# Kernel tuning notes

Hardware: AMD Instinct MI355X
Metric: run time of the kernel (lower is better)

Reference implementation:

```python
import jax, jax.numpy as jnp
import numpy as np

P, N, D, H, AN, F = 20000, 16, 128, 8, 5, 512
DH = D // H  # 16


def layer_norm(x, g, b, eps=1e-5):
    m = jnp.mean(x, axis=-1, keepdims=True)
    v = jnp.var(x, axis=-1, keepdims=True)
    return (x - m) / jnp.sqrt(v + eps) * g + b


def setup_inputs() -> dict:
    key = jax.random.key(0)
    ks = jax.random.split(key, 12)
    s = 0.02
    return {
        "tgt": jax.random.normal(ks[0], (P, D * AN), jnp.float32),
        "index_pair": jax.random.randint(ks[1], (P, N), 0, P, jnp.int64),
        "cnt": P,
        "dist_atten": jax.random.normal(ks[2], (P, N, H), jnp.float32),
        "Wq": jax.random.normal(ks[3], (D, D), jnp.float32) * s,
        "Wk": jax.random.normal(ks[4], (D, D), jnp.float32) * s,
        "Wo": jax.random.normal(ks[5], (D, D), jnp.float32) * s,
        "W1": jax.random.normal(ks[6], (F, D), jnp.float32) * s,
        "b1f": jnp.zeros((F,), jnp.float32),
        "W2": jax.random.normal(ks[7], (D, F), jnp.float32) * s,
        "b2f": jnp.zeros((D,), jnp.float32),
        "g1": jnp.ones((D,), jnp.float32),
        "be1": jnp.zeros((D,), jnp.float32),
        "g2": jnp.ones((D,), jnp.float32),
        "be2": jnp.zeros((D,), jnp.float32),
    }


def reference(tgt, index_pair, cnt, dist_atten, Wq, Wk, Wo, W1, b1f, W2, b2f, g1, be1, g2, be2):
    x = tgt.reshape(P, D, AN)                       # [P, D, an]
    # Linear applied along D (torch Linear: y = x W^T), acting per equivariant channel an
    q = jnp.einsum('pea,de->pda', x, Wq)
    k = jnp.einsum('pea,de->pda', x, Wk)
    v = jnp.einsum('pea,de->pda', x, Wq)            # source uses to_q for value (faithful)
    # irregular neighbor gather (sa_attention_mapper_v3)
    kg = k.reshape(P, D * AN)[index_pair].reshape(P, N, H, DH, AN)
    vg = v.reshape(P, D * AN)[index_pair].reshape(P, N, H, DH, AN)
    qh = q.reshape(P, H, DH, AN)
    dot = jnp.einsum('phdi,pnhdi->pnh', qh, kg)     # [P, N, H]
    att = jax.nn.softmax((dot + dist_atten) / np.sqrt(DH).astype(np.float32), axis=1)
    t2 = jnp.einsum('pnh,pnhci->phci', att, vg).reshape(P, D, AN)
    t2 = jnp.einsum('pea,de->pda', t2, Wo)
    y = (x + t2).transpose(0, 2, 1)                 # [P, an, D]
    y = layer_norm(y, g1, be1)
    ff = jnp.maximum(y @ W1.T + b1f, 0.0) @ W2.T + b2f
    y = layer_norm(y + ff, g2, be2)
    return y.transpose(0, 2, 1).reshape(P, D * AN)
```

## Files before the change

### kernel.cpp

```cpp
#include <hip/hip_runtime.h>

#define PP   20000
#define NN   16
#define DD   128
#define HH   8
#define ANC  5
#define FF   512
#define PD   640
#define ROWS (PP * ANC)
#define SEG  20480


typedef __attribute__((ext_vector_type(8))) short  bf8;
typedef __attribute__((ext_vector_type(8))) unsigned short ushort8;
typedef __attribute__((ext_vector_type(4))) unsigned short us4;
typedef __attribute__((ext_vector_type(4))) float  f32x4;

__device__ inline float bf2f(unsigned short u) {
  union { unsigned int i; float f; } v; v.i = ((unsigned int)u) << 16; return v.f;
}
__device__ inline unsigned short f2bf(float f) {
  union { float f; unsigned int i; } v; v.f = f;
  unsigned int r = v.i + 0x7FFFu + ((v.i >> 16) & 1u);
  return (unsigned short)(r >> 16);
}

__global__ void k_wconv(const float* __restrict__ Wo, const float* __restrict__ W1,
                        const float* __restrict__ W2, const float* __restrict__ Wq,
                        const float* __restrict__ Wk,
                        unsigned short* __restrict__ Wob, unsigned short* __restrict__ W1b,
                        unsigned short* __restrict__ W2b, unsigned short* __restrict__ Wqb,
                        unsigned short* __restrict__ Wkb)
{
  int i = blockIdx.x * 256 + threadIdx.x;
  if (i < 16384) { Wob[i] = f2bf(Wo[i]); Wqb[i] = f2bf(Wq[i]); Wkb[i] = f2bf(Wk[i]); }
  if (i < 65536) { W1b[i] = f2bf(W1[i]); W2b[i] = f2bf(W2[i]); }
}

__global__ __launch_bounds__(320) void k_xpose(
    const float* __restrict__ tgt, unsigned short* __restrict__ xb)
{
  __shared__ float xs[5 * 1032];
  const int t = threadIdx.x;
  const int p0 = blockIdx.x * 8;
  const float* src = tgt + (size_t)p0 * PD;
#pragma unroll
  for (int i = 0; i < 16; ++i) {
    int lin = t + i * 320;
    float v = src[lin];
    int pt = lin / PD;
    int rem = lin - pt * PD;
    int e = rem / 5;
    int a = rem - e * 5;
    xs[a * 1032 + e * 8 + pt] = v;
  }
  __syncthreads();
  const size_t base = (size_t)(blockIdx.x >> 1) * SEG + (size_t)(blockIdx.x & 1) * 5120;
  for (int i = t; i < 5120; i += 320) {
    int row_l = i >> 7, col = i & 127;
    int pt = row_l / 5, a = row_l - pt * 5;
    xb[base + i] = f2bf(xs[a * 1032 + col * 8 + pt]);
  }
}

__global__ __launch_bounds__(256) void k_qk_gemm(
    const unsigned short* __restrict__ xb, const unsigned short* __restrict__ Wqb,
    const unsigned short* __restrict__ Wkb, unsigned char* __restrict__ kq8,
    unsigned short* __restrict__ qb16)
{
  __shared__ unsigned short Sb[80 * 136];
  const int t = threadIdx.x;
  const int w = t >> 6, l = t & 63;
  const int lc = l & 15, kg = l >> 4;
  const int p0 = blockIdx.x * 16;
  const unsigned short* xseg = xb + (size_t)blockIdx.x * SEG;

  f32x4 zq[5][2], zk[5][2];
#pragma unroll
  for (int m = 0; m < 5; ++m)
#pragma unroll
    for (int n = 0; n < 2; ++n) {
      zq[m][n] = (f32x4){0.f, 0.f, 0.f, 0.f};
      zk[m][n] = (f32x4){0.f, 0.f, 0.f, 0.f};
    }
  bf8 wq[2][4], wk[2][4];
#pragma unroll
  for (int nt = 0; nt < 2; ++nt)
#pragma unroll
    for (int kf = 0; kf < 4; ++kf) {
      size_t wo = (size_t)((2 * w + nt) * 16 + lc) * DD + kf * 32 + kg * 8;
      wq[nt][kf] = *reinterpret_cast<const bf8*>(&Wqb[wo]);
      wk[nt][kf] = *reinterpret_cast<const bf8*>(&Wkb[wo]);
    }
#pragma unroll
  for (int mt = 0; mt < 5; ++mt) {
    const unsigned short* ap = xseg + (mt * 16 + lc) * DD + kg * 8;
    bf8 a0 = *reinterpret_cast<const bf8*>(ap);
    bf8 a1 = *reinterpret_cast<const bf8*>(ap + 32);
    bf8 a2 = *reinterpret_cast<const bf8*>(ap + 64);
    bf8 a3 = *reinterpret_cast<const bf8*>(ap + 96);
#pragma unroll
    for (int nt = 0; nt < 2; ++nt) {
      zq[mt][nt] = __builtin_amdgcn_mfma_f32_16x16x32_bf16(a0, wq[nt][0], zq[mt][nt], 0, 0, 0);
      zq[mt][nt] = __builtin_amdgcn_mfma_f32_16x16x32_bf16(a1, wq[nt][1], zq[mt][nt], 0, 0, 0);
      zq[mt][nt] = __builtin_amdgcn_mfma_f32_16x16x32_bf16(a2, wq[nt][2], zq[mt][nt], 0, 0, 0);
      zq[mt][nt] = __builtin_amdgcn_mfma_f32_16x16x32_bf16(a3, wq[nt][3], zq[mt][nt], 0, 0, 0);
      zk[mt][nt] = __builtin_amdgcn_mfma_f32_16x16x32_bf16(a0, wk[nt][0], zk[mt][nt], 0, 0, 0);
      zk[mt][nt] = __builtin_amdgcn_mfma_f32_16x16x32_bf16(a1, wk[nt][1], zk[mt][nt], 0, 0, 0);
      zk[mt][nt] = __builtin_amdgcn_mfma_f32_16x16x32_bf16(a2, wk[nt][2], zk[mt][nt], 0, 0, 0);
      zk[mt][nt] = __builtin_amdgcn_mfma_f32_16x16x32_bf16(a3, wk[nt][3], zk[mt][nt], 0, 0, 0);
    }
  }
#pragma unroll
  for (int mt = 0; mt < 5; ++mt)
#pragma unroll
    for (int j = 0; j < 4; ++j)
#pragma unroll
      for (int nt = 0; nt < 2; ++nt)
        Sb[(mt * 16 + kg * 4 + j) * 136 + (2 * w + nt) * 16 + lc] = f2bf(zq[mt][nt][j]);
  __syncthreads();
  for (int i = t * 4; i < 10240; i += 1024) {
    int pl = i / 640, rem = i - pl * 640;
    unsigned short u[4]; float f[4];
#pragma unroll
    for (int j = 0; j < 4; ++j) {
      int o = rem + j; int d = o / 5, a = o - d * 5;
      u[j] = Sb[(pl * 5 + a) * 136 + d];
      f[j] = bf2f(u[j]);
    }
    us4 uv = {u[0], u[1], u[2], u[3]};
    *reinterpret_cast<us4*>(&qb16[(size_t)(p0 + pl) * 640 + rem]) = uv;
    int wd = 0;
    wd = __builtin_amdgcn_cvt_pk_fp8_f32(f[0], f[1], wd, false);
    wd = __builtin_amdgcn_cvt_pk_fp8_f32(f[2], f[3], wd, true);
    *reinterpret_cast<int*>(&kq8[(size_t)(p0 + pl) * 1280 + 640 + rem]) = wd;
  }
  __syncthreads();
#pragma unroll
  for (int mt = 0; mt < 5; ++mt)
#pragma unroll
    for (int j = 0; j < 4; ++j)
#pragma unroll
      for (int nt = 0; nt < 2; ++nt)
        Sb[(mt * 16 + kg * 4 + j) * 136 + (2 * w + nt) * 16 + lc] = f2bf(zk[mt][nt][j]);
  __syncthreads();
  for (int i = t * 4; i < 10240; i += 1024) {
    int pl = i / 640, rem = i - pl * 640;
    float f[4];
#pragma unroll
    for (int j = 0; j < 4; ++j) {
      int o = rem + j; int d = o / 5, a = o - d * 5;
      f[j] = bf2f(Sb[(pl * 5 + a) * 136 + d]);
    }
    int wd = 0;
    wd = __builtin_amdgcn_cvt_pk_fp8_f32(f[0], f[1], wd, false);
    wd = __builtin_amdgcn_cvt_pk_fp8_f32(f[2], f[3], wd, true);
    *reinterpret_cast<int*>(&kq8[(size_t)(p0 + pl) * 1280 + rem]) = wd;
  }
}

__global__ __launch_bounds__(256, 6) void k_attn(
    const unsigned char* __restrict__ kq8, const unsigned short* __restrict__ qb16,
    const int* __restrict__ idx, const float* __restrict__ dist,
    unsigned short* __restrict__ t2b)
{
  __shared__ unsigned short qsh[640];
  __shared__ float sc[128];
  __shared__ float att[128];
  __shared__ int sidx[NN];
  const int t = threadIdx.x;
  const int p = blockIdx.x;
  if (t < NN) sidx[t] = idx[p * NN + t];
  if (t < 80)
    *reinterpret_cast<ushort8*>(&qsh[t * 8]) =
        *reinterpret_cast<const ushort8*>(&qb16[(size_t)p * 640 + t * 8]);
  float dv = 0.f;
  if (t < 128) dv = dist[(size_t)p * 128 + (t & 15) * 8 + (t >> 4)];
  __syncthreads();
  unsigned vbits[16];
  const int o0 = (t < 160) ? t * 4 : 0;
  if (t < 160) {
#pragma unroll
    for (int n = 0; n < 16; ++n)
      vbits[n] = *reinterpret_cast<const unsigned*>(
          &kq8[(size_t)sidx[n] * 1280 + 640 + o0]);
  }
  if (t < 128) {
    int n = t & 15, h = t >> 4;
    const unsigned char* kp = &kq8[(size_t)sidx[n] * 1280 + h * 80];
    const unsigned short* qp = &qsh[h * 80];
    float acc = 0.f;
#pragma unroll
    for (int j4 = 0; j4 < 5; ++j4) {
      uint4 kw = *reinterpret_cast<const uint4*>(kp + j4 * 16);
      ushort8 qa = *reinterpret_cast<const ushort8*>(qp + j4 * 16);
      ushort8 qb = *reinterpret_cast<const ushort8*>(qp + j4 * 16 + 8);
      acc += __builtin_amdgcn_cvt_f32_fp8(kw.x, 0) * bf2f(qa[0]);
      acc += __builtin_amdgcn_cvt_f32_fp8(kw.x, 1) * bf2f(qa[1]);
      acc += __builtin_amdgcn_cvt_f32_fp8(kw.x, 2) * bf2f(qa[2]);
      acc += __builtin_amdgcn_cvt_f32_fp8(kw.x, 3) * bf2f(qa[3]);
      acc += __builtin_amdgcn_cvt_f32_fp8(kw.y, 0) * bf2f(qa[4]);
      acc += __builtin_amdgcn_cvt_f32_fp8(kw.y, 1) * bf2f(qa[5]);
      acc += __builtin_amdgcn_cvt_f32_fp8(kw.y, 2) * bf2f(qa[6]);
      acc += __builtin_amdgcn_cvt_f32_fp8(kw.y, 3) * bf2f(qa[7]);
      acc += __builtin_amdgcn_cvt_f32_fp8(kw.z, 0) * bf2f(qb[0]);
      acc += __builtin_amdgcn_cvt_f32_fp8(kw.z, 1) * bf2f(qb[1]);
      acc += __builtin_amdgcn_cvt_f32_fp8(kw.z, 2) * bf2f(qb[2]);
      acc += __builtin_amdgcn_cvt_f32_fp8(kw.z, 3) * bf2f(qb[3]);
      acc += __builtin_amdgcn_cvt_f32_fp8(kw.w, 0) * bf2f(qb[4]);
      acc += __builtin_amdgcn_cvt_f32_fp8(kw.w, 1) * bf2f(qb[5]);
      acc += __builtin_amdgcn_cvt_f32_fp8(kw.w, 2) * bf2f(qb[6]);
      acc += __builtin_amdgcn_cvt_f32_fp8(kw.w, 3) * bf2f(qb[7]);
    }
    sc[h * 16 + n] = (acc + dv) * 0.25f;
  }
  __syncthreads();
  if (t < 8) {
    float m = -1e30f;
#pragma unroll
    for (int n = 0; n < 16; ++n) m = fmaxf(m, sc[t * 16 + n]);
    float s = 0.f;
    float ev[16];
#pragma unroll
    for (int n = 0; n < 16; ++n) { ev[n] = __expf(sc[t * 16 + n] - m); s += ev[n]; }
    float inv = 1.f / s;
#pragma unroll
    for (int n = 0; n < 16; ++n) att[t * 16 + n] = ev[n] * inv;
  }
  __syncthreads();
  if (t < 160) {
    const int h = o0 / 80;
    float facc[4] = {0.f, 0.f, 0.f, 0.f};
#pragma unroll
    for (int n = 0; n < 16; ++n) {
      float aw = att[h * 16 + n];
      facc[0] += aw * __builtin_amdgcn_cvt_f32_fp8(vbits[n], 0);
      facc[1] += aw * __builtin_amdgcn_cvt_f32_fp8(vbits[n], 1);
      facc[2] += aw * __builtin_amdgcn_cvt_f32_fp8(vbits[n], 2);
      facc[3] += aw * __builtin_amdgcn_cvt_f32_fp8(vbits[n], 3);
    }
    unsigned short* t2p = t2b + (size_t)(p >> 4) * SEG + 10240 + ((p & 15) * 5) * 128;
#pragma unroll
    for (int j = 0; j < 4; ++j) {
      int o = o0 + j;
      int e = o / 5, a = o - e * 5;
      t2p[a * 128 + e] = f2bf(facc[j]);
    }
  }
}

__global__ __launch_bounds__(256, 2) void k_ffn_mfma(
    float* out, const unsigned short* __restrict__ Wob,
    const unsigned short* __restrict__ W1b, const float* __restrict__ b1,
    const unsigned short* __restrict__ W2b, const float* __restrict__ b2,
    const float* __restrict__ g1, const float* __restrict__ be1,
    const float* __restrict__ g2, const float* __restrict__ be2)
{
  __shared__ unsigned short SH[2 * 80 * 136];
  __shared__ float mrow[80], rrow[80];
  unsigned short* Yb = SH;
  unsigned short* Hb = SH + 80 * 136;
  const int t = threadIdx.x;
  const int w = t >> 6, l = t & 63;
  const int lc = l & 15;
  const int kg = l >> 4;
  const int c0 = (2 * w) * 16 + lc;
  const int c1 = c0 + 16;
  const unsigned short* xseg = (const unsigned short*)out + (size_t)blockIdx.x * SEG;
  const unsigned short* t2seg = xseg + 10240;

  f32x4 zac[5][2];
#pragma unroll
  for (int m = 0; m < 5; ++m)
#pragma unroll
    for (int n = 0; n < 2; ++n) zac[m][n] = (f32x4){0.f, 0.f, 0.f, 0.f};

  {
    bf8 wb[2][4];
#pragma unroll
    for (int nt = 0; nt < 2; ++nt)
#pragma unroll
      for (int kf = 0; kf < 4; ++kf)
        wb[nt][kf] = *reinterpret_cast<const bf8*>(
            &Wob[(size_t)((2 * w + nt) * 16 + lc) * DD + kf * 32 + kg * 8]);
#pragma unroll
    for (int mt = 0; mt < 5; ++mt) {
      const unsigned short* ap = t2seg + (mt * 16 + lc) * DD + kg * 8;
      bf8 a0 = *reinterpret_cast<const bf8*>(ap);
      bf8 a1 = *reinterpret_cast<const bf8*>(ap + 32);
      bf8 a2 = *reinterpret_cast<const bf8*>(ap + 64);
      bf8 a3 = *reinterpret_cast<const bf8*>(ap + 96);
#pragma unroll
      for (int nt = 0; nt < 2; ++nt) {
        zac[mt][nt] = __builtin_amdgcn_mfma_f32_16x16x32_bf16(a0, wb[nt][0], zac[mt][nt], 0, 0, 0);
        zac[mt][nt] = __builtin_amdgcn_mfma_f32_16x16x32_bf16(a1, wb[nt][1], zac[mt][nt], 0, 0, 0);
        zac[mt][nt] = __builtin_amdgcn_mfma_f32_16x16x32_bf16(a2, wb[nt][2], zac[mt][nt], 0, 0, 0);
        zac[mt][nt] = __builtin_amdgcn_mfma_f32_16x16x32_bf16(a3, wb[nt][3], zac[mt][nt], 0, 0, 0);
      }
    }
  }
#pragma unroll
  for (int mt = 0; mt < 5; ++mt) {
    int rb = mt * 16 + kg * 4;
#pragma unroll
    for (int j = 0; j < 4; ++j) {
      int row = rb + j;
      zac[mt][0][j] += bf2f(xseg[row * DD + c0]);
      zac[mt][1][j] += bf2f(xseg[row * DD + c1]);
      Yb[row * 136 + c0] = f2bf(zac[mt][0][j]);
      Yb[row * 136 + c1] = f2bf(zac[mt][1][j]);
    }
  }
  __syncthreads();
  if (t < 160) {
    int row = t >> 1, hf = t & 1;
    const unsigned short* rp = Yb + row * 136 + hf * 64;
    float s = 0.f, s2 = 0.f;
#pragma unroll
    for (int c8 = 0; c8 < 8; ++c8) {
      bf8 v8 = *reinterpret_cast<const bf8*>(rp + c8 * 8);
#pragma unroll
      for (int j = 0; j < 8; ++j) {
        float f = bf2f((unsigned short)v8[j]);
        s += f; s2 += f * f;
      }
    }
    s += __shfl_xor(s, 1); s2 += __shfl_xor(s2, 1);
    if (!hf) {
      float mm = s * (1.f / 128.f);
      float vv = s2 * (1.f / 128.f) - mm * mm;
      mrow[row] = mm;
      rrow[row] = rsqrtf(vv + 1e-5f);
    }
  }
  __syncthreads();
  {
    float g1a = g1[c0], g1b = g1[c1], e1a = be1[c0], e1b = be1[c1];
#pragma unroll
    for (int mt = 0; mt < 5; ++mt) {
      int rb = mt * 16 + kg * 4;
#pragma unroll
      for (int j = 0; j < 4; ++j) {
        int row = rb + j;
        float mm = mrow[row], rr = rrow[row];
        float y0 = (zac[mt][0][j] - mm) * rr * g1a + e1a;
        float y1 = (zac[mt][1][j] - mm) * rr * g1b + e1b;
        zac[mt][0][j] = y0; zac[mt][1][j] = y1;
        Yb[row * 136 + c0] = f2bf(y0);
        Yb[row * 136 + c1] = f2bf(y1);
      }
    }
  }
  __syncthreads();
  f32x4 oac[5][2];
#pragma unroll
  for (int m = 0; m < 5; ++m)
#pragma unroll
    for (int n = 0; n < 2; ++n) oac[m][n] = (f32x4){0.f, 0.f, 0.f, 0.f};

  for (int c = 0; c < 4; ++c) {
    bf8 w1f[2][4];
#pragma unroll
    for (int nt = 0; nt < 2; ++nt)
#pragma unroll
      for (int kf = 0; kf < 4; ++kf)
        w1f[nt][kf] = *reinterpret_cast<const bf8*>(
            &W1b[(size_t)(c * 128 + (2 * w + nt) * 16 + lc) * DD + kf * 32 + kg * 8]);
    f32x4 hac[5][2];
#pragma unroll
    for (int m = 0; m < 5; ++m)
#pragma unroll
      for (int n = 0; n < 2; ++n) hac[m][n] = (f32x4){0.f, 0.f, 0.f, 0.f};
#pragma unroll
    for (int mt = 0; mt < 5; ++mt) {
      const unsigned short* yp = Yb + (mt * 16 + lc) * 136 + kg * 8;
      bf8 a0 = *reinterpret_cast<const bf8*>(yp);
      bf8 a1 = *reinterpret_cast<const bf8*>(yp + 32);
      bf8 a2 = *reinterpret_cast<const bf8*>(yp + 64);
      bf8 a3 = *reinterpret_cast<const bf8*>(yp + 96);
#pragma unroll
      for (int nt = 0; nt < 2; ++nt) {
        hac[mt][nt] = __builtin_amdgcn_mfma_f32_16x16x32_bf16(a0, w1f[nt][0], hac[mt][nt], 0, 0, 0);
        hac[mt][nt] = __builtin_amdgcn_mfma_f32_16x16x32_bf16(a1, w1f[nt][1], hac[mt][nt], 0, 0, 0);
        hac[mt][nt] = __builtin_amdgcn_mfma_f32_16x16x32_bf16(a2, w1f[nt][2], hac[mt][nt], 0, 0, 0);
        hac[mt][nt] = __builtin_amdgcn_mfma_f32_16x16x32_bf16(a3, w1f[nt][3], hac[mt][nt], 0, 0, 0);
      }
    }
    float b1a = b1[c * 128 + c0], b1b = b1[c * 128 + c1];
    __syncthreads();
#pragma unroll
    for (int mt = 0; mt < 5; ++mt) {
      int rb = mt * 16 + kg * 4;
#pragma unroll
      for (int j = 0; j < 4; ++j) {
        int row = rb + j;
        Hb[row * 136 + c0] = f2bf(fmaxf(hac[mt][0][j] + b1a, 0.f));
        Hb[row * 136 + c1] = f2bf(fmaxf(hac[mt][1][j] + b1b, 0.f));
      }
    }
    __syncthreads();
    bf8 w2f[2][4];
#pragma unroll
    for (int nt = 0; nt < 2; ++nt)
#pragma unroll
      for (int kf = 0; kf < 4; ++kf)
        w2f[nt][kf] = *reinterpret_cast<const bf8*>(
            &W2b[(size_t)((2 * w + nt) * 16 + lc) * FF + c * 128 + kf * 32 + kg * 8]);
#pragma unroll
    for (int mt = 0; mt < 5; ++mt) {
      const unsigned short* hp = Hb + (mt * 16 + lc) * 136 + kg * 8;
      bf8 a0 = *reinterpret_cast<const bf8*>(hp);
      bf8 a1 = *reinterpret_cast<const bf8*>(hp + 32);
      bf8 a2 = *reinterpret_cast<const bf8*>(hp + 64);
      bf8 a3 = *reinterpret_cast<const bf8*>(hp + 96);
#pragma unroll
      for (int nt = 0; nt < 2; ++nt) {
        oac[mt][nt] = __builtin_amdgcn_mfma_f32_16x16x32_bf16(a0, w2f[nt][0], oac[mt][nt], 0, 0, 0);
        oac[mt][nt] = __builtin_amdgcn_mfma_f32_16x16x32_bf16(a1, w2f[nt][1], oac[mt][nt], 0, 0, 0);
        oac[mt][nt] = __builtin_amdgcn_mfma_f32_16x16x32_bf16(a2, w2f[nt][2], oac[mt][nt], 0, 0, 0);
        oac[mt][nt] = __builtin_amdgcn_mfma_f32_16x16x32_bf16(a3, w2f[nt][3], oac[mt][nt], 0, 0, 0);
      }
    }
  }
  __syncthreads();
  {
    float b2a = b2[c0], b2b = b2[c1];
#pragma unroll
    for (int mt = 0; mt < 5; ++mt) {
      int rb = mt * 16 + kg * 4;
#pragma unroll
      for (int j = 0; j < 4; ++j) {
        int row = rb + j;
        float v0 = zac[mt][0][j] + oac[mt][0][j] + b2a;
        float v1 = zac[mt][1][j] + oac[mt][1][j] + b2b;
        oac[mt][0][j] = v0; oac[mt][1][j] = v1;
        Yb[row * 136 + c0] = f2bf(v0);
        Yb[row * 136 + c1] = f2bf(v1);
      }
    }
  }
  __syncthreads();
  if (t < 160) {
    int row = t >> 1, hf = t & 1;
    const unsigned short* rp = Yb + row * 136 + hf * 64;
    float s = 0.f, s2 = 0.f;
#pragma unroll
    for (int c8 = 0; c8 < 8; ++c8) {
      bf8 v8 = *reinterpret_cast<const bf8*>(rp + c8 * 8);
#pragma unroll
      for (int j = 0; j < 8; ++j) {
        float f = bf2f((unsigned short)v8[j]);
        s += f; s2 += f * f;
      }
    }
    s += __shfl_xor(s, 1); s2 += __shfl_xor(s2, 1);
    if (!hf) {
      float mm = s * (1.f / 128.f);
      float vv = s2 * (1.f / 128.f) - mm * mm;
      mrow[row] = mm;
      rrow[row] = rsqrtf(vv + 1e-5f);
    }
  }
  __syncthreads();
  {
    float* fb = (float*)SH;
    float g2a = g2[c0], g2b = g2[c1], e2a = be2[c0], e2b = be2[c1];
#pragma unroll
    for (int mt = 0; mt < 5; ++mt) {
      int rb = mt * 16 + kg * 4;
#pragma unroll
      for (int j = 0; j < 4; ++j) {
        int row = rb + j;
        float mm = mrow[row], rr = rrow[row];
        fb[row * 132 + c0] = (oac[mt][0][j] - mm) * rr * g2a + e2a;
        fb[row * 132 + c1] = (oac[mt][1][j] - mm) * rr * g2b + e2b;
      }
    }
    __syncthreads();
    const size_t ob = (size_t)blockIdx.x * 16 * PD;
    for (int i = t; i < 10240; i += 256) {
      int pl = i / PD, rem = i - pl * PD;
      int d = rem / 5, a = rem - d * 5;
      out[ob + i] = fb[(pl * 5 + a) * 132 + d];
    }
  }
}

extern "C" void kernel_launch(void* const* d_in, const int* in_sizes, int n_in,
                              void* d_out, int out_size, void* d_ws, size_t ws_size,
                              hipStream_t stream) {
  (void)in_sizes; (void)n_in; (void)out_size; (void)ws_size;
  const float* tgt  = (const float*)d_in[0];
  const int*   idx  = (const int*)d_in[1];
  const float* dist = (const float*)d_in[3];
  const float* Wq   = (const float*)d_in[4];
  const float* Wk   = (const float*)d_in[5];
  const float* Wo   = (const float*)d_in[6];
  const float* W1   = (const float*)d_in[7];
  const float* b1f  = (const float*)d_in[8];
  const float* W2   = (const float*)d_in[9];
  const float* b2f  = (const float*)d_in[10];
  const float* g1   = (const float*)d_in[11];
  const float* be1  = (const float*)d_in[12];
  const float* g2   = (const float*)d_in[13];
  const float* be2  = (const float*)d_in[14];
  float* out = (float*)d_out;

  unsigned char*  kq8  = (unsigned char*)d_ws;
  unsigned short* qb16 = (unsigned short*)(kq8 + (size_t)PP * 1280);
  unsigned short* Wob  = qb16 + (size_t)PP * 640;
  unsigned short* W1b  = Wob + DD * DD;
  unsigned short* W2b  = W1b + FF * DD;
  unsigned short* Wqb  = W2b + FF * DD;
  unsigned short* Wkb  = Wqb + DD * DD;
  unsigned short* ovl  = (unsigned short*)d_out;

  k_wconv  <<<256, 256, 0, stream>>>(Wo, W1, W2, Wq, Wk, Wob, W1b, W2b, Wqb, Wkb);
  k_xpose  <<<PP / 8, 320, 0, stream>>>(tgt, ovl);
  k_qk_gemm<<<ROWS / 80, 256, 0, stream>>>(ovl, Wqb, Wkb, kq8, qb16);
  k_attn   <<<PP, 256, 0, stream>>>(kq8, qb16, idx, dist, ovl);
  k_ffn_mfma<<<ROWS / 80, 256, 0, stream>>>(out, Wob, W1b, b1f, W2b, b2f,
                                            g1, be1, g2, be2);
}
```

Measured before the change: 316.6 us.

## Swap MFMA operands so accumulators hold contiguous features and raise occupancy hint

The FFN kernel's MFMA calls now pass the weight tiles as the A operand and the activation tiles as B. Each lane's four accumulator values then cover four consecutive feature columns of one row. This lets the epilogues (residual add, layernorm, bias/ReLU, output staging) use packed 4-wide LDS stores, vector global loads, and float4 parameter loads instead of scalar 2-byte stores. Launch bounds also go from 2 to 3 blocks per CU, which limits registers per thread and risks spills given the large accumulator arrays.

```diff
diff --git a/kernel.cpp b/kernel.cpp
--- a/kernel.cpp
+++ b/kernel.cpp
@@ -249,7 +249,7 @@
   }
 }
 
-__global__ __launch_bounds__(256, 2) void k_ffn_mfma(
+__global__ __launch_bounds__(256, 3) void k_ffn_mfma(
     float* out, const unsigned short* __restrict__ Wob,
     const unsigned short* __restrict__ W1b, const float* __restrict__ b1,
     const unsigned short* __restrict__ W2b, const float* __restrict__ b2,
@@ -264,51 +264,52 @@
   const int w = t >> 6, l = t & 63;
   const int lc = l & 15;
   const int kg = l >> 4;
-  const int c0 = (2 * w) * 16 + lc;
-  const int c1 = c0 + 16;
+  const int d0 = w * 32 + kg * 4;
   const unsigned short* xseg = (const unsigned short*)out + (size_t)blockIdx.x * SEG;
   const unsigned short* t2seg = xseg + 10240;
 
-  f32x4 zac[5][2];
-#pragma unroll
-  for (int m = 0; m < 5; ++m)
-#pragma unroll
-    for (int n = 0; n < 2; ++n) zac[m][n] = (f32x4){0.f, 0.f, 0.f, 0.f};
+  f32x4 zac[2][5];
+#pragma unroll
+  for (int m = 0; m < 2; ++m)
+#pragma unroll
+    for (int n = 0; n < 5; ++n) zac[m][n] = (f32x4){0.f, 0.f, 0.f, 0.f};
 
   {
     bf8 wb[2][4];
 #pragma unroll
-    for (int nt = 0; nt < 2; ++nt)
+    for (int mi = 0; mi < 2; ++mi)
 #pragma unroll
       for (int kf = 0; kf < 4; ++kf)
-        wb[nt][kf] = *reinterpret_cast<const bf8*>(
-            &Wob[(size_t)((2 * w + nt) * 16 + lc) * DD + kf * 32 + kg * 8]);
-#pragma unroll
-    for (int mt = 0; mt < 5; ++mt) {
-      const unsigned short* ap = t2seg + (mt * 16 + lc) * DD + kg * 8;
-      bf8 a0 = *reinterpret_cast<const bf8*>(ap);
-      bf8 a1 = *reinterpret_cast<const bf8*>(ap + 32);
-      bf8 a2 = *reinterpret_cast<const bf8*>(ap + 64);
-      bf8 a3 = *reinterpret_cast<const bf8*>(ap + 96);
-#pragma unroll
-      for (int nt = 0; nt < 2; ++nt) {
-        zac[mt][nt] = __builtin_amdgcn_mfma_f32_16x16x32_bf16(a0, wb[nt][0], zac[mt][nt], 0, 0, 0);
-        zac[mt][nt] = __builtin_amdgcn_mfma_f32_16x16x32_bf16(a1, wb[nt][1], zac[mt][nt], 0, 0, 0);
-        zac[mt][nt] = __builtin_amdgcn_mfma_f32_16x16x32_bf16(a2, wb[nt][2], zac[mt][nt], 0, 0, 0);
-        zac[mt][nt] = __builtin_amdgcn_mfma_f32_16x16x32_bf16(a3, wb[nt][3], zac[mt][nt], 0, 0, 0);
-      }
-    }
-  }
-#pragma unroll
-  for (int mt = 0; mt < 5; ++mt) {
-    int rb = mt * 16 + kg * 4;
-#pragma unroll
-    for (int j = 0; j < 4; ++j) {
-      int row = rb + j;
-      zac[mt][0][j] += bf2f(xseg[row * DD + c0]);
-      zac[mt][1][j] += bf2f(xseg[row * DD + c1]);
-      Yb[row * 136 + c0] = f2bf(zac[mt][0][j]);
-      Yb[row * 136 + c1] = f2bf(zac[mt][1][j]);
+        wb[mi][kf] = *reinterpret_cast<const bf8*>(
+            &Wob[(size_t)((2 * w + mi) * 16 + lc) * DD + kf * 32 + kg * 8]);
+#pragma unroll
+    for (int ni = 0; ni < 5; ++ni) {
+      const unsigned short* bp = t2seg + (ni * 16 + lc) * DD + kg * 8;
+      bf8 b0 = *reinterpret_cast<const bf8*>(bp);
+      bf8 b1v = *reinterpret_cast<const bf8*>(bp + 32);
+      bf8 b2v = *reinterpret_cast<const bf8*>(bp + 64);
+      bf8 b3 = *reinterpret_cast<const bf8*>(bp + 96);
+#pragma unroll
+      for (int mi = 0; mi < 2; ++mi) {
+        zac[mi][ni] = __builtin_amdgcn_mfma_f32_16x16x32_bf16(wb[mi][0], b0, zac[mi][ni], 0, 0, 0);
+        zac[mi][ni] = __builtin_amdgcn_mfma_f32_16x16x32_bf16(wb[mi][1], b1v, zac[mi][ni], 0, 0, 0);
+        zac[mi][ni] = __builtin_amdgcn_mfma_f32_16x16x32_bf16(wb[mi][2], b2v, zac[mi][ni], 0, 0, 0);
+        zac[mi][ni] = __builtin_amdgcn_mfma_f32_16x16x32_bf16(wb[mi][3], b3, zac[mi][ni], 0, 0, 0);
+      }
+    }
+  }
+#pragma unroll
+  for (int mi = 0; mi < 2; ++mi) {
+    int dd = d0 + mi * 16;
+#pragma unroll
+    for (int ni = 0; ni < 5; ++ni) {
+      int r = ni * 16 + lc;
+      us4 x4 = *reinterpret_cast<const us4*>(&xseg[r * DD + dd]);
+#pragma unroll
+      for (int j = 0; j < 4; ++j) zac[mi][ni][j] += bf2f(x4[j]);
+      us4 pk = {f2bf(zac[mi][ni][0]), f2bf(zac[mi][ni][1]),
+                f2bf(zac[mi][ni][2]), f2bf(zac[mi][ni][3])};
+      *reinterpret_cast<us4*>(&Yb[r * 136 + dd]) = pk;
     }
   }
   __syncthreads();
@@ -335,107 +336,127 @@
   }
   __syncthreads();
   {
-    float g1a = g1[c0], g1b = g1[c1], e1a = be1[c0], e1b = be1[c1];
-#pragma unroll
-    for (int mt = 0; mt < 5; ++mt) {
-      int rb = mt * 16 + kg * 4;
-#pragma unroll
-      for (int j = 0; j < 4; ++j) {
-        int row = rb + j;
-        float mm = mrow[row], rr = rrow[row];
-        float y0 = (zac[mt][0][j] - mm) * rr * g1a + e1a;
-        float y1 = (zac[mt][1][j] - mm) * rr * g1b + e1b;
-        zac[mt][0][j] = y0; zac[mt][1][j] = y1;
-        Yb[row * 136 + c0] = f2bf(y0);
-        Yb[row * 136 + c1] = f2bf(y1);
-      }
-    }
-  }
-  __syncthreads();
-  f32x4 oac[5][2];
-#pragma unroll
-  for (int m = 0; m < 5; ++m)
-#pragma unroll
-    for (int n = 0; n < 2; ++n) oac[m][n] = (f32x4){0.f, 0.f, 0.f, 0.f};
+    float4 gv[2], ev[2];
+#pragma unroll
+    for (int mi = 0; mi < 2; ++mi) {
+      gv[mi] = *reinterpret_cast<const float4*>(&g1[d0 + mi * 16]);
+      ev[mi] = *reinterpret_cast<const float4*>(&be1[d0 + mi * 16]);
+    }
+#pragma unroll
+    for (int mi = 0; mi < 2; ++mi) {
+      int dd = d0 + mi * 16;
+      float ga[4] = {gv[mi].x, gv[mi].y, gv[mi].z, gv[mi].w};
+      float ea[4] = {ev[mi].x, ev[mi].y, ev[mi].z, ev[mi].w};
+#pragma unroll
+      for (int ni = 0; ni < 5; ++ni) {
+        int r = ni * 16 + lc;
+        float mm = mrow[r], rr = rrow[r];
+#pragma unroll
+        for (int j = 0; j < 4; ++j)
+          zac[mi][ni][j] = (zac[mi][ni][j] - mm) * rr * ga[j] + ea[j];
+        us4 pk = {f2bf(zac[mi][ni][0]), f2bf(zac[mi][ni][1]),
+                  f2bf(zac[mi][ni][2]), f2bf(zac[mi][ni][3])};
+        *reinterpret_cast<us4*>(&Yb[r * 136 + dd]) = pk;
+      }
+    }
+  }
+  __syncthreads();
+  f32x4 oac[2][5];
+#pragma unroll
+  for (int m = 0; m < 2; ++m)
+#pragma unroll
+    for (int n = 0; n < 5; ++n) oac[m][n] = (f32x4){0.f, 0.f, 0.f, 0.f};
 
   for (int c = 0; c < 4; ++c) {
     bf8 w1f[2][4];
 #pragma unroll
-    for (int nt = 0; nt < 2; ++nt)
+    for (int mi = 0; mi < 2; ++mi)
 #pragma unroll
       for (int kf = 0; kf < 4; ++kf)
-        w1f[nt][kf] = *reinterpret_cast<const bf8*>(
-            &W1b[(size_t)(c * 128 + (2 * w + nt) * 16 + lc) * DD + kf * 32 + kg * 8]);
-    f32x4 hac[5][2];
-#pragma unroll
-    for (int m = 0; m < 5; ++m)
-#pragma unroll
-      for (int n = 0; n < 2; ++n) hac[m][n] = (f32x4){0.f, 0.f, 0.f, 0.f};
-#pragma unroll
-    for (int mt = 0; mt < 5; ++mt) {
-      const unsigned short* yp = Yb + (mt * 16 + lc) * 136 + kg * 8;
-      bf8 a0 = *reinterpret_cast<const bf8*>(yp);
-      bf8 a1 = *reinterpret_cast<const bf8*>(yp + 32);
-      bf8 a2 = *reinterpret_cast<const bf8*>(yp + 64);
-      bf8 a3 = *reinterpret_cast<const bf8*>(yp + 96);
-#pragma unroll
-      for (int nt = 0; nt < 2; ++nt) {
-        hac[mt][nt] = __builtin_amdgcn_mfma_f32_16x16x32_bf16(a0, w1f[nt][0], hac[mt][nt], 0, 0, 0);
-        hac[mt][nt] = __builtin_amdgcn_mfma_f32_16x16x32_bf16(a1, w1f[nt][1], hac[mt][nt], 0, 0, 0);
-        hac[mt][nt] = __builtin_amdgcn_mfma_f32_16x16x32_bf16(a2, w1f[nt][2], hac[mt][nt], 0, 0, 0);
-        hac[mt][nt] = __builtin_amdgcn_mfma_f32_16x16x32_bf16(a3, w1f[nt][3], hac[mt][nt], 0, 0, 0);
-      }
-    }
-    float b1a = b1[c * 128 + c0], b1b = b1[c * 128 + c1];
+        w1f[mi][kf] = *reinterpret_cast<const bf8*>(
+            &W1b[(size_t)(c * 128 + (2 * w + mi) * 16 + lc) * DD + kf * 32 + kg * 8]);
+    f32x4 hac[2][5];
+#pragma unroll
+    for (int m = 0; m < 2; ++m)
+#pragma unroll
+      for (int n = 0; n < 5; ++n) hac[m][n] = (f32x4){0.f, 0.f, 0.f, 0.f};
+#pragma unroll
+    for (int ni = 0; ni < 5; ++ni) {
+      const unsigned short* bp = Yb + (ni * 16 + lc) * 136 + kg * 8;
+      bf8 b0 = *reinterpret_cast<const bf8*>(bp);
+      bf8 b1v = *reinterpret_cast<const bf8*>(bp + 32);
+      bf8 b2v = *reinterpret_cast<const bf8*>(bp + 64);
+      bf8 b3 = *reinterpret_cast<const bf8*>(bp + 96);
+#pragma unroll
+      for (int mi = 0; mi < 2; ++mi) {
+        hac[mi][ni] = __builtin_amdgcn_mfma_f32_16x16x32_bf16(w1f[mi][0], b0, hac[mi][ni], 0, 0, 0);
+        hac[mi][ni] = __builtin_amdgcn_mfma_f32_16x16x32_bf16(w1f[mi][1], b1v, hac[mi][ni], 0, 0, 0);
+        hac[mi][ni] = __builtin_amdgcn_mfma_f32_16x16x32_bf16(w1f[mi][2], b2v, hac[mi][ni], 0, 0, 0);
+        hac[mi][ni] = __builtin_amdgcn_mfma_f32_16x16x32_bf16(w1f[mi][3], b3, hac[mi][ni], 0, 0, 0);
+      }
+    }
+    float4 bb[2];
+#pragma unroll
+    for (int mi = 0; mi < 2; ++mi)
+      bb[mi] = *reinterpret_cast<const float4*>(&b1[c * 128 + d0 + mi * 16]);
     __syncthreads();
 #pragma unroll
-    for (int mt = 0; mt < 5; ++mt) {
-      int rb = mt * 16 + kg * 4;
-#pragma unroll
-      for (int j = 0; j < 4; ++j) {
-        int row = rb + j;
-        Hb[row * 136 + c0] = f2bf(fmaxf(hac[mt][0][j] + b1a, 0.f));
-        Hb[row * 136 + c1] = f2bf(fmaxf(hac[mt][1][j] + b1b, 0.f));
+    for (int mi = 0; mi < 2; ++mi) {
+      int dd = d0 + mi * 16;
+      float ba[4] = {bb[mi].x, bb[mi].y, bb[mi].z, bb[mi].w};
+#pragma unroll
+      for (int ni = 0; ni < 5; ++ni) {
+        int r = ni * 16 + lc;
+        us4 pk = {f2bf(fmaxf(hac[mi][ni][0] + ba[0], 0.f)),
+                  f2bf(fmaxf(hac[mi][ni][1] + ba[1], 0.f)),
+                  f2bf(fmaxf(hac[mi][ni][2] + ba[2], 0.f)),
+                  f2bf(fmaxf(hac[mi][ni][3] + ba[3], 0.f))};
+        *reinterpret_cast<us4*>(&Hb[r * 136 + dd]) = pk;
       }
     }
     __syncthreads();
     bf8 w2f[2][4];
 #pragma unroll
-    for (int nt = 0; nt < 2; ++nt)
+    for (int mi = 0; mi < 2; ++mi)
 #pragma unroll
       for (int kf = 0; kf < 4; ++kf)
-        w2f[nt][kf] = *reinterpret_cast<const bf8*>(
-            &W2b[(size_t)((2 * w + nt) * 16 + lc) * FF + c * 128 + kf * 32 + kg * 8]);
-#pragma unroll
-    for (int mt = 0; mt < 5; ++mt) {
-      const unsigned short* hp = Hb + (mt * 16 + lc) * 136 + kg * 8;
-      bf8 a0 = *reinterpret_cast<const bf8*>(hp);
-      bf8 a1 = *reinterpret_cast<const bf8*>(hp + 32);
-      bf8 a2 = *reinterpret_cast<const bf8*>(hp + 64);
-      bf8 a3 = *reinterpret_cast<const bf8*>(hp + 96);
-#pragma unroll
-      for (int nt = 0; nt < 2; ++nt) {
-        oac[mt][nt] = __builtin_amdgcn_mfma_f32_16x16x32_bf16(a0, w2f[nt][0], oac[mt][nt], 0, 0, 0);
-        oac[mt][nt] = __builtin_amdgcn_mfma_f32_16x16x32_bf16(a1, w2f[nt][1], oac[mt][nt], 0, 0, 0);
-        oac[mt][nt] = __builtin_amdgcn_mfma_f32_16x16x32_bf16(a2, w2f[nt][2], oac[mt][nt], 0, 0, 0);
-        oac[mt][nt] = __builtin_amdgcn_mfma_f32_16x16x32_bf16(a3, w2f[nt][3], oac[mt][nt], 0, 0, 0);
+        w2f[mi][kf] = *reinterpret_cast<const bf8*>(
+            &W2b[(size_t)((2 * w + mi) * 16 + lc) * FF + c * 128 + kf * 32 + kg * 8]);
+#pragma unroll
+    for (int ni = 0; ni < 5; ++ni) {
+      const unsigned short* bp = Hb + (ni * 16 + lc) * 136 + kg * 8;
+      bf8 b0 = *reinterpret_cast<const bf8*>(bp);
+      bf8 b1v = *reinterpret_cast<const bf8*>(bp + 32);
+      bf8 b2v = *reinterpret_cast<const bf8*>(bp + 64);
+      bf8 b3 = *reinterpret_cast<const bf8*>(bp + 96);
+#pragma unroll
+      for (int mi = 0; mi < 2; ++mi) {
+        oac[mi][ni] = __builtin_amdgcn_mfma_f32_16x16x32_bf16(w2f[mi][0], b0, oac[mi][ni], 0, 0, 0);
+        oac[mi][ni] = __builtin_amdgcn_mfma_f32_16x16x32_bf16(w2f[mi][1], b1v, oac[mi][ni], 0, 0, 0);
+        oac[mi][ni] = __builtin_amdgcn_mfma_f32_16x16x32_bf16(w2f[mi][2], b2v, oac[mi][ni], 0, 0, 0);
+        oac[mi][ni] = __builtin_amdgcn_mfma_f32_16x16x32_bf16(w2f[mi][3], b3, oac[mi][ni], 0, 0, 0);
       }
     }
   }
   __syncthreads();
   {
-    float b2a = b2[c0], b2b = b2[c1];
-#pragma unroll
-    for (int mt = 0; mt < 5; ++mt) {
-      int rb = mt * 16 + kg * 4;
-#pragma unroll
-      for (int j = 0; j < 4; ++j) {
-        int row = rb + j;
-        float v0 = zac[mt][0][j] + oac[mt][0][j] + b2a;
-        float v1 = zac[mt][1][j] + oac[mt][1][j] + b2b;
-        oac[mt][0][j] = v0; oac[mt][1][j] = v1;
-        Yb[row * 136 + c0] = f2bf(v0);
-        Yb[row * 136 + c1] = f2bf(v1);
+    float4 b2v4[2];
+#pragma unroll
+    for (int mi = 0; mi < 2; ++mi)
+      b2v4[mi] = *reinterpret_cast<const float4*>(&b2[d0 + mi * 16]);
+#pragma unroll
+    for (int mi = 0; mi < 2; ++mi) {
+      int dd = d0 + mi * 16;
+      float ba[4] = {b2v4[mi].x, b2v4[mi].y, b2v4[mi].z, b2v4[mi].w};
+#pragma unroll
+      for (int ni = 0; ni < 5; ++ni) {
+        int r = ni * 16 + lc;
+#pragma unroll
+        for (int j = 0; j < 4; ++j)
+          oac[mi][ni][j] += zac[mi][ni][j] + ba[j];
+        us4 pk = {f2bf(oac[mi][ni][0]), f2bf(oac[mi][ni][1]),
+                  f2bf(oac[mi][ni][2]), f2bf(oac[mi][ni][3])};
+        *reinterpret_cast<us4*>(&Yb[r * 136 + dd]) = pk;
       }
     }
   }
@@ -464,16 +485,26 @@
   __syncthreads();
   {
     float* fb = (float*)SH;
-    float g2a = g2[c0], g2b = g2[c1], e2a = be2[c0], e2b = be2[c1];
-#pragma unroll
-    for (int mt = 0; mt < 5; ++mt) {
-      int rb = mt * 16 + kg * 4;
-#pragma unroll
-      for (int j = 0; j < 4; ++j) {
-        int row = rb + j;
-        float mm = mrow[row], rr = rrow[row];
-        fb[row * 132 + c0] = (oac[mt][0][j] - mm) * rr * g2a + e2a;
-        fb[row * 132 + c1] = (oac[mt][1][j] - mm) * rr * g2b + e2b;
+    float4 gv[2], ev[2];
+#pragma unroll
+    for (int mi = 0; mi < 2; ++mi) {
+      gv[mi] = *reinterpret_cast<const float4*>(&g2[d0 + mi * 16]);
+      ev[mi] = *reinterpret_cast<const float4*>(&be2[d0 + mi * 16]);
+    }
+#pragma unroll
+    for (int mi = 0; mi < 2; ++mi) {
+      int dd = d0 + mi * 16;
+      float ga[4] = {gv[mi].x, gv[mi].y, gv[mi].z, gv[mi].w};
+      float ea[4] = {ev[mi].x, ev[mi].y, ev[mi].z, ev[mi].w};
+#pragma unroll
+      for (int ni = 0; ni < 5; ++ni) {
+        int r = ni * 16 + lc;
+        float mm = mrow[r], rr = rrow[r];
+        f32x4 o;
+#pragma unroll
+        for (int j = 0; j < 4; ++j)
+          o[j] = (oac[mi][ni][j] - mm) * rr * ga[j] + ea[j];
+        *reinterpret_cast<f32x4*>(&fb[r * 132 + dd]) = o;
       }
     }
     __syncthreads();
```

New measurement: 318.1 us. Within noise of the previous version (+0.5%).
